# Kernel optimization log

Hardware: AMD Instinct MI355X
Metric: run time of the kernel (lower is better)

## Reference

```python
import jax, jax.numpy as jnp
import numpy as np

B, T, E, H, V = 32, 256, 1024, 1024, 32000


def setup_inputs() -> dict:
    key = jax.random.key(0)
    ks = jax.random.split(key, 6)
    s = 0.02  # initrange-style scale
    return {
        "words": jax.random.randint(ks[0], (B, T), 0, V),
        "embed_w": jax.random.normal(ks[1], (V, E), dtype=jnp.float32) * s,
        "w_ih": jax.random.normal(ks[2], (4 * H, E), dtype=jnp.float32) * s,
        "w_hh": jax.random.normal(ks[3], (4 * H, H), dtype=jnp.float32) * s,
        "b_ih": jnp.zeros((4 * H,), jnp.float32),
        "b_hh": jnp.zeros((4 * H,), jnp.float32),
        "emit_w": jax.random.normal(ks[4], (V, H), dtype=jnp.float32) * s,
        "emit_b": jnp.zeros((V,), jnp.float32),
    }


def _lstm_cell(x, h, c, w_ih, w_hh, b_ih, b_hh):
    # PyTorch LSTMCell gate order: i, f, g, o
    gates = x @ w_ih.T + b_ih + h @ w_hh.T + b_hh  # [B, 4H]
    i, f, g, o = jnp.split(gates, 4, axis=-1)
    i = jax.nn.sigmoid(i)
    f = jax.nn.sigmoid(f)
    g = jnp.tanh(g)
    o = jax.nn.sigmoid(o)
    c_new = f * c + i * g
    h_new = o * jnp.tanh(c_new)
    return h_new, c_new


def reference(words, embed_w, w_ih, w_hh, b_ih, b_hh, emit_w, emit_b):
    emb = embed_w[words]  # [B, T, E]
    h0 = jnp.zeros((B, H), emb.dtype)
    c0 = jnp.zeros((B, H), emb.dtype)

    def step(carry, xs):
        h, c = carry
        x_t, w_t = xs  # x_t: [B,E], w_t: [B]
        h, c = _lstm_cell(x_t, h, c, w_ih, w_hh, b_ih, b_hh)
        logits = h @ emit_w.T + emit_b          # [B, V]
        logp = jax.nn.log_softmax(logits, -1)   # [B, V]
        ll = jnp.take_along_axis(logp, w_t[:, None], axis=1)[:, 0]  # [B]
        return (h, c), ll

    xs = (jnp.swapaxes(emb, 0, 1), jnp.swapaxes(words, 0, 1))  # time-major
    _, emit_ll = jax.lax.scan(step, (h0, c0), xs)
    return emit_ll  # [T, B] per-token log-likelihoods
```

## Files before the change

kernel.cpp:

```cpp
#include <hip/hip_runtime.h>
#include <stdint.h>

#define B_ 32
#define T_ 256
#define E_ 1024
#define H_ 1024
#define V_ 32000

typedef unsigned short u16;
typedef unsigned int   u32;
typedef unsigned long long u64;

typedef __attribute__((ext_vector_type(8))) short bf16x8;
typedef __attribute__((ext_vector_type(4))) float f32x4;

__device__ __forceinline__ float bf2f(u16 u){ u32 x = ((u32)u) << 16; return __uint_as_float(x); }
__device__ __forceinline__ u16  f2bf(float f){
  u32 x = __float_as_uint(f);
  u32 r = (x + 0x7fffu + ((x >> 16) & 1u)) >> 16;
  return (u16)r;
}
__device__ __forceinline__ float fsig(float x){ return 1.f / (1.f + __expf(-x)); }
__device__ __forceinline__ float ftanh(float x){
  float e = __expf(2.f * x);
  return 1.f - 2.f / (e + 1.f);
}

__device__ __forceinline__ void gload_lds16(const void* g, void* l){
  __builtin_amdgcn_global_load_lds((const __attribute__((address_space(1))) unsigned int*)g,
                                   (__attribute__((address_space(3))) unsigned int*)l, 16, 0, 0);
}

__global__ void k_prep_wc(const float* __restrict__ wih, const float* __restrict__ whh,
                          u16* __restrict__ Wc){
  int i = blockIdx.x * 256 + threadIdx.x;
  int r = i >> 9; int k4 = (i & 511) << 2;
  const float* src = (k4 < 1024) ? (wih + (size_t)r * 1024 + k4)
                                 : (whh + (size_t)r * 1024 + (k4 - 1024));
  float4 v = *(const float4*)src;
  u64 pk = (u64)f2bf(v.x) | ((u64)f2bf(v.y) << 16) | ((u64)f2bf(v.z) << 32) | ((u64)f2bf(v.w) << 48);
  *(u64*)(Wc + (size_t)r * 2048 + k4) = pk;
}

__global__ void k_prep_ew(const float* __restrict__ src, u16* __restrict__ dst){
  size_t i = (size_t)(blockIdx.x * 256 + threadIdx.x) * 4;
  float4 v = *(const float4*)(src + i);
  u64 pk = (u64)f2bf(v.x) | ((u64)f2bf(v.y) << 16) | ((u64)f2bf(v.z) << 32) | ((u64)f2bf(v.w) << 48);
  *(u64*)(dst + i) = pk;
}

__global__ void k_prep_bsum(const float* __restrict__ bih, const float* __restrict__ bhh,
                            float* __restrict__ bsum){
  int i = blockIdx.x * 256 + threadIdx.x;
  bsum[i] = bih[i] + bhh[i];
}

__global__ void k_gather_x(const int* __restrict__ words, const float* __restrict__ embed,
                           u16* __restrict__ X){
  int row = blockIdx.x;
  int t = row >> 5, b = row & 31;
  int wd = words[b * T_ + t];
  const float* src = embed + (size_t)wd * E_;
  u16* dst = X + (size_t)row * E_;
  int e = threadIdx.x * 4;
  float4 v = *(const float4*)(src + e);
  u64 pk = (u64)f2bf(v.x) | ((u64)f2bf(v.y) << 16) | ((u64)f2bf(v.z) << 32) | ((u64)f2bf(v.w) << 48);
  *(u64*)(dst + e) = pk;
}

__device__ __forceinline__ void tile_gemm(const u16* __restrict__ Ab, const u16* __restrict__ Bb,
                                          int blog2, char* sm, f32x4 (&acc)[4][4],
                                          int tid, int lane, int wr, int wc){
  char* As = sm;
  char* Bs = sm + 16384;
  for (int kk = 0; kk < 32; ++kk){
    {
      int u0 = tid;
      int r0 = u0 >> 2, s0 = (u0 & 3) ^ ((r0 >> 1) & 3);
      gload_lds16(Ab + (((size_t)r0) << 10) + kk * 32 + s0 * 8, As + (size_t)u0 * 16);
      int u1 = 512 + tid;
      int r1 = u1 >> 2, s1 = (u1 & 3) ^ ((r1 >> 1) & 3);
      gload_lds16(Ab + (((size_t)r1) << 10) + kk * 32 + s1 * 8, As + (size_t)u1 * 16);
      int r2 = tid >> 2, s2 = (tid & 3) ^ ((r2 >> 1) & 3);
      gload_lds16(Bb + (((size_t)r2) << blog2) + kk * 32 + s2 * 8, Bs + (size_t)tid * 16);
    }
    __syncthreads();
    bf16x8 af[4], bfr[4];
    #pragma unroll
    for (int mi = 0; mi < 4; ++mi){
      int r = wr * 64 + mi * 16 + (lane & 15);
      u32 byte = ((u32)r << 6) + (((u32)lane >> 4) << 4);
      byte ^= (u32)(r & 6) << 3;
      af[mi] = *(const bf16x8*)(As + byte);
    }
    #pragma unroll
    for (int ni = 0; ni < 4; ++ni){
      int r = wc * 64 + ni * 16 + (lane & 15);
      u32 byte = ((u32)r << 6) + (((u32)lane >> 4) << 4);
      byte ^= (u32)(r & 6) << 3;
      bfr[ni] = *(const bf16x8*)(Bs + byte);
    }
    #pragma unroll
    for (int mi = 0; mi < 4; ++mi)
      #pragma unroll
      for (int ni = 0; ni < 4; ++ni)
        acc[mi][ni] = __builtin_amdgcn_mfma_f32_16x16x32_bf16(af[mi], bfr[ni], acc[mi][ni], 0, 0, 0);
    __syncthreads();
  }
}

__launch_bounds__(512, 2)
__global__ void k_xgemm(const u16* __restrict__ X, const u16* __restrict__ Wc,
                        const float* __restrict__ bsum, u16* __restrict__ Xg){
  __shared__ __align__(16) char smem[24576];
  const int tid = threadIdx.x, lane = tid & 63, w = tid >> 6;
  const int wr = w >> 1, wc = w & 1;
  const int mtx = blockIdx.x >> 5, vcx = blockIdx.x & 31;
  const u16* Ab = X + (size_t)mtx * 256 * 1024;
  const u16* Bb = Wc + (size_t)vcx * 128 * 2048;
  f32x4 acc[4][4];
  #pragma unroll
  for (int mi = 0; mi < 4; ++mi)
    #pragma unroll
    for (int ni = 0; ni < 4; ++ni){ f32x4 z = {0.f,0.f,0.f,0.f}; acc[mi][ni] = z; }
  tile_gemm(Ab, Bb, 11, smem, acc, tid, lane, wr, wc);
  float bcol[4];
  #pragma unroll
  for (int ni = 0; ni < 4; ++ni)
    bcol[ni] = bsum[vcx * 128 + wc * 64 + ni * 16 + (lane & 15)];
  int colb = vcx * 128 + wc * 64 + (lane & 15);
  int rowb = mtx * 256 + wr * 64 + ((lane >> 4) << 2);
  #pragma unroll
  for (int mi = 0; mi < 4; ++mi){
    #pragma unroll
    for (int ni = 0; ni < 4; ++ni){
      float b = bcol[ni];
      u32 lo = (u32)f2bf(acc[mi][ni][0] + b) | ((u32)f2bf(acc[mi][ni][1] + b) << 16);
      u32 hi = (u32)f2bf(acc[mi][ni][2] + b) | ((u32)f2bf(acc[mi][ni][3] + b) << 16);
      uint2 pk; pk.x = lo; pk.y = hi;
      *(uint2*)(Xg + (size_t)(colb + ni * 16) * 8192 + rowb + mi * 16) = pk;
    }
  }
}

__device__ __forceinline__ void emit_tile(int qi, const u16* __restrict__ Hall,
                                          const u16* __restrict__ Ew,
                                          const float* __restrict__ emit_b,
                                          float* __restrict__ parts,
                                          u32* __restrict__ flags,
                                          char* sm, int tid, int lane, int w){
  u32 mt = (u32)qi / 250u, vc = (u32)qi % 250u;
  int wr = w >> 1, wc = w & 1;
  if (w == 0){
    u32 tgtv = mt * 8u + 8u;
    u32 budget = 1u << 20;
    const u32* fp = flags + (lane << 5);
    for (;;){
      u32 fv;
      asm volatile("global_load_dword %0, %1, off sc0 sc1\n\ts_waitcnt vmcnt(0)"
                   : "=v"(fv) : "v"(fp) : "memory");
      if (__all((int)(fv >= tgtv)) || !--budget) break;
      __builtin_amdgcn_s_sleep(16);
    }
  }
  __syncthreads();
  const u16* Ab = Hall + 32 * 1024 + (size_t)mt * 256 * 1024;
  const u16* Bb = Ew + (size_t)vc * 128 * 1024;
  f32x4 acc[4][4];
  #pragma unroll
  for (int mi = 0; mi < 4; ++mi)
    #pragma unroll
    for (int ni = 0; ni < 4; ++ni){ f32x4 z = {0.f,0.f,0.f,0.f}; acc[mi][ni] = z; }
  tile_gemm(Ab, Bb, 10, sm, acc, tid, lane, wr, wc);
  float* rs = (float*)(sm + 24576);
  float eb[4];
  #pragma unroll
  for (int ni = 0; ni < 4; ++ni)
    eb[ni] = emit_b[vc * 128 + wc * 64 + ni * 16 + (lane & 15)];
  #pragma unroll
  for (int mi = 0; mi < 4; ++mi){
    #pragma unroll
    for (int r = 0; r < 4; ++r){
      float s = 0.f;
      #pragma unroll
      for (int ni = 0; ni < 4; ++ni) s += __expf(acc[mi][ni][r] + eb[ni]);
      s += __shfl_xor(s, 1); s += __shfl_xor(s, 2); s += __shfl_xor(s, 4); s += __shfl_xor(s, 8);
      if ((lane & 15) == 0)
        rs[wc * 256 + wr * 64 + mi * 16 + ((lane >> 4) << 2) + r] = s;
    }
  }
  __syncthreads();
  if (tid < 256)
    parts[(size_t)vc * 8192 + (size_t)mt * 256 + tid] = rs[tid] + rs[256 + tid];
  __syncthreads();
}

__launch_bounds__(512, 2)
__global__ void k_mega(const u16* __restrict__ Wc, const u16* __restrict__ Xg,
                       const u16* __restrict__ Ew, const float* __restrict__ emit_b,
                       u16* __restrict__ Hall, float* __restrict__ parts,
                       u32* __restrict__ ctrl){
  __shared__ __align__(16) char smem[65536];
  __shared__ int qshare;
  u32* q2    = ctrl;
  u32* flags = ctrl + 1024;

  const int tid  = threadIdx.x;
  const int lane = tid & 63;
  const int w    = tid >> 6;
  const int bid  = blockIdx.x;

  if (bid >= 64){
    for (;;){
      if (tid == 0) qshare = (int)__hip_atomic_fetch_add(q2, 1u, __ATOMIC_RELAXED, __HIP_MEMORY_SCOPE_AGENT);
      __syncthreads();
      int qi = qshare;
      __syncthreads();
      if (qi >= 8000) break;
      emit_tile(qi, Hall, Ew, emit_b, parts, flags, smem, tid, lane, w);
    }
    return;
  }

  const int nc0  = bid << 4;
  const int em   = tid >> 4, en = tid & 15;
  const int arow = lane & 15;
  const int akg  = (lane >> 4) << 3;
  float c = 0.f;
  float* Gp = (float*)smem;

  bf16x8 breg[4][4];
  {
    const u16* bp = Wc + (((size_t)(nc0 + arow)) << 11) + 1024 + (w << 7) + akg;
    #pragma unroll
    for (int g = 0; g < 4; ++g)
      #pragma unroll
      for (int kk = 0; kk < 4; ++kk)
        breg[g][kk] = *(const bf16x8*)(bp + (((size_t)g) << 21) + (kk << 5));
  }

  const u16* xgb = Xg + (size_t)(nc0 + en) * 8192 + em;

  for (int t = 0; t < T_; ++t){
    {
      const u32* fp = flags + ((8 * w + (lane & 7)) << 5);
      u32 budget = 1u << 22;
      u32 fv;
      do {
        asm volatile("global_load_dword %0, %1, off sc0 sc1\n\ts_waitcnt vmcnt(0)"
                     : "=v"(fv) : "v"(fp) : "memory");
      } while (!__all((int)(fv >= (u32)t)) && --budget);
    }
    uint4 a0[4], a1[4];
    {
      const u16* h0 = Hall + (((size_t)t) << 15) + (((size_t)arow) << 10) + (w << 7) + akg;
      const u16* h1 = h0 + 16384;
      #pragma unroll
      for (int kk = 0; kk < 4; ++kk){
        asm volatile("global_load_dwordx4 %0, %1, off offset:%2 sc0 sc1"
                     : "=v"(a0[kk]) : "v"(h0), "n"(kk * 64));
        asm volatile("global_load_dwordx4 %0, %1, off offset:%2 sc0 sc1"
                     : "=v"(a1[kk]) : "v"(h1), "n"(kk * 64));
      }
    }
    u16 x0 = xgb[(size_t)t * 32];
    u16 x1 = xgb[1024ull * 8192 + (size_t)t * 32];
    u16 x2 = xgb[2048ull * 8192 + (size_t)t * 32];
    u16 x3 = xgb[3072ull * 8192 + (size_t)t * 32];
    asm volatile("s_waitcnt vmcnt(0)" ::: "memory");
    __builtin_amdgcn_sched_barrier(0);

    f32x4 acc[4][2];
    #pragma unroll
    for (int g = 0; g < 4; ++g){ f32x4 z = {0.f,0.f,0.f,0.f}; acc[g][0] = z; acc[g][1] = z; }
    #pragma unroll
    for (int kk = 0; kk < 4; ++kk){
      bf16x8 f0 = __builtin_bit_cast(bf16x8, a0[kk]);
      bf16x8 f1 = __builtin_bit_cast(bf16x8, a1[kk]);
      #pragma unroll
      for (int g = 0; g < 4; ++g){
        acc[g][0] = __builtin_amdgcn_mfma_f32_16x16x32_bf16(f0, breg[g][kk], acc[g][0], 0, 0, 0);
        acc[g][1] = __builtin_amdgcn_mfma_f32_16x16x32_bf16(f1, breg[g][kk], acc[g][1], 0, 0, 0);
      }
    }
    #pragma unroll
    for (int g = 0; g < 4; ++g)
      #pragma unroll
      for (int mt2 = 0; mt2 < 2; ++mt2)
        #pragma unroll
        for (int r = 0; r < 4; ++r){
          int m = ((lane >> 4) << 2) + r + mt2 * 16;
          Gp[((w * 4 + g) * 32 + m) * 16 + (lane & 15)] = acc[g][mt2][r];
        }
    __syncthreads();

    {
      float s0 = bf2f(x0), s1 = bf2f(x1), s2 = bf2f(x2), s3 = bf2f(x3);
      #pragma unroll
      for (int p = 0; p < 8; ++p){
        s0 += Gp[((p * 4 + 0) * 32 + em) * 16 + en];
        s1 += Gp[((p * 4 + 1) * 32 + em) * 16 + en];
        s2 += Gp[((p * 4 + 2) * 32 + em) * 16 + en];
        s3 += Gp[((p * 4 + 3) * 32 + em) * 16 + en];
      }
      float ig = fsig(s0), fg = fsig(s1), gg = ftanh(s2), og = fsig(s3);
      c = fg * c + ig * gg;
      float h = og * ftanh(c);
      u32 hb = (u32)f2bf(h);
      const u16* hp = Hall + (((size_t)(t + 1)) << 15) + (((size_t)em) << 10) + nc0 + en;
      asm volatile("global_store_short %0, %1, off sc0 sc1" :: "v"(hp), "v"(hb) : "memory");
    }
    asm volatile("s_waitcnt vmcnt(0)" ::: "memory");
    __syncthreads();
    if (tid == 0){
      u32 fv = (u32)(t + 1);
      asm volatile("global_store_dword %0, %1, off sc0 sc1"
                   :: "v"(flags + (bid << 5)), "v"(fv) : "memory");
    }
  }

  for (;;){
    if (tid == 0) qshare = (int)__hip_atomic_fetch_add(q2, 1u, __ATOMIC_RELAXED, __HIP_MEMORY_SCOPE_AGENT);
    __syncthreads();
    int qi = qshare;
    __syncthreads();
    if (qi >= 8000) break;
    emit_tile(qi, Hall, Ew, emit_b, parts, flags, smem, tid, lane, w);
  }
}

__global__ void k_target(const u16* __restrict__ Hall, const u16* __restrict__ Ew,
                         const int* __restrict__ words, const float* __restrict__ emit_b,
                         float* __restrict__ tgt){
  int row  = blockIdx.x * 4 + (threadIdx.x >> 6);
  int lane = threadIdx.x & 63;
  int t = row >> 5, b = row & 31;
  int wd = words[b * T_ + t];
  const bf16x8* ha = (const bf16x8*)(Hall + (size_t)(row + 32) * 1024 + lane * 16);
  const bf16x8* wa = (const bf16x8*)(Ew + (size_t)wd * 1024 + lane * 16);
  float s = 0.f;
  #pragma unroll
  for (int p = 0; p < 2; ++p){
    bf16x8 av = ha[p], wv = wa[p];
    #pragma unroll
    for (int i = 0; i < 8; ++i) s += bf2f((u16)av[i]) * bf2f((u16)wv[i]);
  }
  s += __shfl_xor(s, 32); s += __shfl_xor(s, 16); s += __shfl_xor(s, 8);
  s += __shfl_xor(s, 4);  s += __shfl_xor(s, 2);  s += __shfl_xor(s, 1);
  if (lane == 0) tgt[row] = s + emit_b[wd];
}

__global__ void k_final(const float* __restrict__ partials, const float* __restrict__ tgt,
                        float* __restrict__ out){
  int i = blockIdx.x * 256 + threadIdx.x;
  float s = 0.f;
  for (int vcb = 0; vcb < 250; ++vcb) s += partials[(size_t)vcb * 8192 + i];
  out[i] = tgt[i] - logf(s);
}

extern "C" void kernel_launch(void* const* d_in, const int* in_sizes, int n_in,
                              void* d_out, int out_size, void* d_ws, size_t ws_size,
                              hipStream_t stream){
  const int*   words = (const int*)d_in[0];
  const float* embed = (const float*)d_in[1];
  const float* wih   = (const float*)d_in[2];
  const float* whh   = (const float*)d_in[3];
  const float* bih   = (const float*)d_in[4];
  const float* bhh   = (const float*)d_in[5];
  const float* emw   = (const float*)d_in[6];
  const float* emb_b = (const float*)d_in[7];
  float* out = (float*)d_out;

  char* ws = (char*)d_ws;
  u16* Wc   = (u16*)ws;
  u16* Ew   = (u16*)(ws + 16777216);
  u16* X    = (u16*)(ws + 82313216);
  u16* Hall = (u16*)(ws + 99090432);
  u16* Xg   = (u16*)(ws + 115933184);
  float* bsum = (float*)(ws + 183042048);
  float* tgt  = (float*)(ws + 183058432);
  float* parts= (float*)(ws + 183091200);
  u32*  ctrl  = (u32*)(ws + 191283200);
  size_t need = 191283200ULL + 16384ULL;
  if (ws_size < need) return;

  hipMemsetAsync(ctrl, 0, 16384, stream);
  hipMemsetAsync(Hall, 0, 32 * 1024 * 2, stream);

  k_prep_wc  <<<8192,  256, 0, stream>>>(wih, whh, Wc);
  k_prep_ew  <<<32000, 256, 0, stream>>>(emw, Ew);
  k_prep_bsum<<<16,    256, 0, stream>>>(bih, bhh, bsum);
  k_gather_x <<<8192,  256, 0, stream>>>(words, embed, X);
  k_xgemm    <<<1024,  512, 0, stream>>>(X, Wc, bsum, Xg);
  k_mega     <<<256,   512, 0, stream>>>(Wc, Xg, Ew, emb_b, Hall, parts, ctrl);
  k_target   <<<2048,  256, 0, stream>>>(Hall, Ew, words, emb_b, tgt);
  k_final    <<<32,    256, 0, stream>>>(parts, tgt, out);
}
```

Measured before the change: 1.497 ms.

## Double-buffer GEMM tiles, per-wave flags, and launch more mega blocks

Double-buffers the LDS tile staging in the shared GEMM helper so the next K-slice loads while the current one is multiplied. The recurrent step now publishes one flag per wave, with no block-wide barrier before the store. Consumers read eight flags with vector loads and take their minimum. The mega kernel launches 512 blocks with a higher occupancy bound and raises wave priority during the recurrence, so emit work can run beside the serial LSTM. The risks are extra LDS per block, lower register budget per wave, and a spin-wait protocol that depends on all flags being visible.

```diff
diff --git a/kernel.cpp b/kernel.cpp
--- a/kernel.cpp
+++ b/kernel.cpp
@@ -25,6 +25,7 @@
   float e = __expf(2.f * x);
   return 1.f - 2.f / (e + 1.f);
 }
+__device__ __forceinline__ u32 umin2(u32 a, u32 b){ return a < b ? a : b; }
 
 __device__ __forceinline__ void gload_lds16(const void* g, void* l){
   __builtin_amdgcn_global_load_lds((const __attribute__((address_space(1))) unsigned int*)g,
@@ -68,23 +69,35 @@
   *(u64*)(dst + e) = pk;
 }
 
+__device__ __forceinline__ void stage_tile(const u16* __restrict__ Ab, const u16* __restrict__ Bb,
+                                           int blog2, char* buf, int kk, int tid){
+  char* As = buf;
+  char* Bs = buf + 16384;
+  int u0 = tid, r0 = u0 >> 2, s0 = (u0 & 3) ^ ((r0 >> 1) & 3);
+  gload_lds16(Ab + (((size_t)r0) << 10) + kk * 32 + s0 * 8, As + (size_t)u0 * 16);
+  int u1 = 512 + tid, r1 = u1 >> 2, s1 = (u1 & 3) ^ ((r1 >> 1) & 3);
+  gload_lds16(Ab + (((size_t)r1) << 10) + kk * 32 + s1 * 8, As + (size_t)u1 * 16);
+  int r2 = tid >> 2, s2 = (tid & 3) ^ ((r2 >> 1) & 3);
+  gload_lds16(Bb + (((size_t)r2) << blog2) + kk * 32 + s2 * 8, Bs + (size_t)tid * 16);
+}
+
 __device__ __forceinline__ void tile_gemm(const u16* __restrict__ Ab, const u16* __restrict__ Bb,
                                           int blog2, char* sm, f32x4 (&acc)[4][4],
                                           int tid, int lane, int wr, int wc){
-  char* As = sm;
-  char* Bs = sm + 16384;
+  stage_tile(Ab, Bb, blog2, sm, 0, tid);
+  #pragma unroll 2
   for (int kk = 0; kk < 32; ++kk){
-    {
-      int u0 = tid;
-      int r0 = u0 >> 2, s0 = (u0 & 3) ^ ((r0 >> 1) & 3);
-      gload_lds16(Ab + (((size_t)r0) << 10) + kk * 32 + s0 * 8, As + (size_t)u0 * 16);
-      int u1 = 512 + tid;
-      int r1 = u1 >> 2, s1 = (u1 & 3) ^ ((r1 >> 1) & 3);
-      gload_lds16(Ab + (((size_t)r1) << 10) + kk * 32 + s1 * 8, As + (size_t)u1 * 16);
-      int r2 = tid >> 2, s2 = (tid & 3) ^ ((r2 >> 1) & 3);
-      gload_lds16(Bb + (((size_t)r2) << blog2) + kk * 32 + s2 * 8, Bs + (size_t)tid * 16);
-    }
-    __syncthreads();
+    char* cur = sm + (size_t)(kk & 1) * 24576;
+    if (kk < 31){
+      stage_tile(Ab, Bb, blog2, sm + (size_t)((kk + 1) & 1) * 24576, kk + 1, tid);
+      asm volatile("s_waitcnt vmcnt(3)" ::: "memory");
+    } else {
+      asm volatile("s_waitcnt vmcnt(0)" ::: "memory");
+    }
+    __builtin_amdgcn_s_barrier();
+    __builtin_amdgcn_sched_barrier(0);
+    char* As = cur;
+    char* Bs = cur + 16384;
     bf16x8 af[4], bfr[4];
     #pragma unroll
     for (int mi = 0; mi < 4; ++mi){
@@ -105,14 +118,14 @@
       #pragma unroll
       for (int ni = 0; ni < 4; ++ni)
         acc[mi][ni] = __builtin_amdgcn_mfma_f32_16x16x32_bf16(af[mi], bfr[ni], acc[mi][ni], 0, 0, 0);
-    __syncthreads();
+    __builtin_amdgcn_s_barrier();
   }
 }
 
 __launch_bounds__(512, 2)
 __global__ void k_xgemm(const u16* __restrict__ X, const u16* __restrict__ Wc,
                         const float* __restrict__ bsum, u16* __restrict__ Xg){
-  __shared__ __align__(16) char smem[24576];
+  __shared__ __align__(16) char smem[49152];
   const int tid = threadIdx.x, lane = tid & 63, w = tid >> 6;
   const int wr = w >> 1, wc = w & 1;
   const int mtx = blockIdx.x >> 5, vcx = blockIdx.x & 31;
@@ -147,19 +160,23 @@
                                           const u16* __restrict__ Ew,
                                           const float* __restrict__ emit_b,
                                           float* __restrict__ parts,
-                                          u32* __restrict__ flags,
+                                          u32* __restrict__ flagw,
                                           char* sm, int tid, int lane, int w){
   u32 mt = (u32)qi / 250u, vc = (u32)qi % 250u;
   int wr = w >> 1, wc = w & 1;
   if (w == 0){
     u32 tgtv = mt * 8u + 8u;
     u32 budget = 1u << 20;
-    const u32* fp = flags + (lane << 5);
+    const u32* fp = flagw + (lane << 5);
     for (;;){
-      u32 fv;
-      asm volatile("global_load_dword %0, %1, off sc0 sc1\n\ts_waitcnt vmcnt(0)"
-                   : "=v"(fv) : "v"(fp) : "memory");
-      if (__all((int)(fv >= tgtv)) || !--budget) break;
+      uint4 f0, f1;
+      asm volatile("global_load_dwordx4 %0, %2, off sc0 sc1\n\t"
+                   "global_load_dwordx4 %1, %2, off offset:16 sc0 sc1\n\t"
+                   "s_waitcnt vmcnt(0)"
+                   : "=v"(f0), "=v"(f1) : "v"(fp) : "memory");
+      u32 mn = umin2(umin2(umin2(f0.x, f0.y), umin2(f0.z, f0.w)),
+                     umin2(umin2(f1.x, f1.y), umin2(f1.z, f1.w)));
+      if (__all((int)(mn >= tgtv)) || !--budget) break;
       __builtin_amdgcn_s_sleep(16);
     }
   }
@@ -172,7 +189,7 @@
     #pragma unroll
     for (int ni = 0; ni < 4; ++ni){ f32x4 z = {0.f,0.f,0.f,0.f}; acc[mi][ni] = z; }
   tile_gemm(Ab, Bb, 10, sm, acc, tid, lane, wr, wc);
-  float* rs = (float*)(sm + 24576);
+  float* rs = (float*)(sm + 49152);
   float eb[4];
   #pragma unroll
   for (int ni = 0; ni < 4; ++ni)
@@ -195,7 +212,7 @@
   __syncthreads();
 }
 
-__launch_bounds__(512, 2)
+__launch_bounds__(512, 4)
 __global__ void k_mega(const u16* __restrict__ Wc, const u16* __restrict__ Xg,
                        const u16* __restrict__ Ew, const float* __restrict__ emit_b,
                        u16* __restrict__ Hall, float* __restrict__ parts,
@@ -203,7 +220,7 @@
   __shared__ __align__(16) char smem[65536];
   __shared__ int qshare;
   u32* q2    = ctrl;
-  u32* flags = ctrl + 1024;
+  u32* flagw = ctrl + 1024;
 
   const int tid  = threadIdx.x;
   const int lane = tid & 63;
@@ -217,11 +234,12 @@
       int qi = qshare;
       __syncthreads();
       if (qi >= 8000) break;
-      emit_tile(qi, Hall, Ew, emit_b, parts, flags, smem, tid, lane, w);
+      emit_tile(qi, Hall, Ew, emit_b, parts, flagw, smem, tid, lane, w);
     }
     return;
   }
 
+  __builtin_amdgcn_s_setprio(1);
   const int nc0  = bid << 4;
   const int em   = tid >> 4, en = tid & 15;
   const int arow = lane & 15;
@@ -243,7 +261,7 @@
 
   for (int t = 0; t < T_; ++t){
     {
-      const u32* fp = flags + ((8 * w + (lane & 7)) << 5);
+      const u32* fp = flagw + ((8 * w + (lane >> 3)) << 5) + (lane & 7);
       u32 budget = 1u << 22;
       u32 fv;
       do {
@@ -269,6 +287,7 @@
     u16 x3 = xgb[3072ull * 8192 + (size_t)t * 32];
     asm volatile("s_waitcnt vmcnt(0)" ::: "memory");
     __builtin_amdgcn_sched_barrier(0);
+    __syncthreads();
 
     f32x4 acc[4][2];
     #pragma unroll
@@ -311,13 +330,13 @@
       asm volatile("global_store_short %0, %1, off sc0 sc1" :: "v"(hp), "v"(hb) : "memory");
     }
     asm volatile("s_waitcnt vmcnt(0)" ::: "memory");
-    __syncthreads();
-    if (tid == 0){
+    if (lane == 0){
       u32 fv = (u32)(t + 1);
       asm volatile("global_store_dword %0, %1, off sc0 sc1"
-                   :: "v"(flags + (bid << 5)), "v"(fv) : "memory");
-    }
-  }
+                   :: "v"(flagw + (bid << 5) + w), "v"(fv) : "memory");
+    }
+  }
+  __builtin_amdgcn_s_setprio(0);
 
   for (;;){
     if (tid == 0) qshare = (int)__hip_atomic_fetch_add(q2, 1u, __ATOMIC_RELAXED, __HIP_MEMORY_SCOPE_AGENT);
@@ -325,7 +344,7 @@
     int qi = qshare;
     __syncthreads();
     if (qi >= 8000) break;
-    emit_tile(qi, Hall, Ew, emit_b, parts, flags, smem, tid, lane, w);
+    emit_tile(qi, Hall, Ew, emit_b, parts, flagw, smem, tid, lane, w);
   }
 }
 
@@ -392,7 +411,7 @@
   k_prep_bsum<<<16,    256, 0, stream>>>(bih, bhh, bsum);
   k_gather_x <<<8192,  256, 0, stream>>>(words, embed, X);
   k_xgemm    <<<1024,  512, 0, stream>>>(X, Wc, bsum, Xg);
-  k_mega     <<<256,   512, 0, stream>>>(Wc, Xg, Ew, emb_b, Hall, parts, ctrl);
+  k_mega     <<<512,   512, 0, stream>>>(Wc, Xg, Ew, emb_b, Hall, parts, ctrl);
   k_target   <<<2048,  256, 0, stream>>>(Hall, Ew, words, emb_b, tgt);
   k_final    <<<32,    256, 0, stream>>>(parts, tgt, out);
 }
```

After: 2.712 ms. +81.1%, slower.
